# Kernel optimization log

Hardware: AMD Instinct MI355X
Metric: run time of the kernel (lower is better)

Reference implementation:

```python
import jax, jax.numpy as jnp
import numpy as np
from jax import lax


def setup_inputs() -> dict:
    key = jax.random.key(0)
    ks = jax.random.split(key, 6)
    B, L, Cin, N, Cout = 4, 4096, 256, 512, 256
    s = 0.02
    return {
        "x": jax.random.normal(ks[0], (B, L, Cin), dtype=jnp.float32),
        "Wx": jax.random.normal(ks[1], (Cin, N), dtype=jnp.float32) * s,
        "bx": jnp.zeros((N,), dtype=jnp.float32),
        "Wbc": jax.random.normal(ks[2], (Cin, 2 * N), dtype=jnp.float32) * s,
        "bbc": jnp.zeros((2 * N,), dtype=jnp.float32),
        "Wd": jax.random.normal(ks[3], (Cin, N), dtype=jnp.float32) * s,
        "bd": jnp.zeros((N,), dtype=jnp.float32),
        "Wy": jax.random.normal(ks[4], (N, Cout), dtype=jnp.float32) * s,
        "by": jnp.zeros((Cout,), dtype=jnp.float32),
    }


def _scan_combine(c1, c2):
    # linear recurrence h_t = a_t * h_{t-1} + b_t as an associative op
    a1, b1 = c1
    a2, b2 = c2
    return a1 * a2, a2 * b1 + b2


def reference(x, Wx, bx, Wbc, bbc, Wd, bd, Wy, by):
    # projections: [B, L, N]
    x_proj = x @ Wx + bx
    BC = x @ Wbc + bbc
    delta = x @ Wd + bd
    Bm, C = jnp.split(BC, 2, axis=-1)

    A_bar = jnp.exp(-jax.nn.softplus(delta))      # [B, L, N], in (0, 1)
    B_bar = (1.0 - A_bar) * Bm                    # [B, L, N]

    # selective scan (h0 = 0): h_t = A_bar_t * h_{t-1} + B_bar_t * x_proj_t
    u = B_bar * x_proj
    _, h = lax.associative_scan(_scan_combine, (A_bar, u), axis=1)

    y = C * h                                      # [B, L, N]
    return y @ Wy + by                             # [B, L, Cout]
```

## Files before the change

kernel.cpp:

```cpp
#include <hip/hip_runtime.h>
#include <math.h>

constexpr int CIN  = 256;
constexpr int NST  = 512;
constexpr int LSEQ = 4096;
constexpr int BB   = 4;
constexpr int ROWS = BB * LSEQ;
constexpr int COUT = 256;
constexpr int LC   = 64;
constexpr int NC   = LSEQ / LC;

typedef __attribute__((ext_vector_type(8))) short bf16x8;
typedef __attribute__((ext_vector_type(4))) float f32x4;
typedef unsigned short ushort_t;
typedef unsigned int   uint_t;

__device__ __forceinline__ ushort_t f2bf(float f) {
    uint_t u = __float_as_uint(f);
    u = (u + 0x7FFF + ((u >> 16) & 1)) >> 16;
    return (ushort_t)u;
}
__device__ __forceinline__ float bf2f(ushort_t s) {
    return __uint_as_float(((uint_t)s) << 16);
}

__global__ __launch_bounds__(256)
void prep_w_kernel(const float* __restrict__ Wx, const float* __restrict__ Wbc,
                   const float* __restrict__ Wd, const float* __restrict__ Wy,
                   ushort_t* __restrict__ Wt, ushort_t* __restrict__ Wyt)
{
    const int gid = blockIdx.x * 256 + threadIdx.x;
    if (gid < 4 * NST * CIN) {
        const int mat = gid >> 17;
        const int idx = gid & 131071;
        const int k   = idx >> 9;
        const int n   = idx & 511;
        float v;
        if      (mat == 0) v = Wx [k * NST + n];
        else if (mat == 1) v = Wbc[k * (2 * NST) + n];
        else if (mat == 2) v = Wbc[k * (2 * NST) + NST + n];
        else               v = Wd [k * NST + n];
        Wt[((size_t)mat * NST + n) * CIN + k] = f2bf(v);
    } else {
        const int idx = gid - 4 * NST * CIN;
        const int k   = idx >> 8;
        const int n   = idx & 255;
        Wyt[(size_t)n * NST + k] = f2bf(Wy[k * COUT + n]);
    }
}

__global__ __launch_bounds__(256)
void prep_x_kernel(const float* __restrict__ x, ushort_t* __restrict__ xb)
{
    const int i = (blockIdx.x * 256 + threadIdx.x) * 4;
    float4 v = *(const float4*)&x[i];
    uint2 o;
    o.x = (uint_t)f2bf(v.x) | ((uint_t)f2bf(v.y) << 16);
    o.y = (uint_t)f2bf(v.z) | ((uint_t)f2bf(v.w) << 16);
    *(uint2*)&xb[i] = o;
}

__global__ __launch_bounds__(256, 3)
void proj_mfma_kernel(const ushort_t* __restrict__ xb, const ushort_t* __restrict__ Wt,
                      const float* __restrict__ bx, const float* __restrict__ bbc,
                      const float* __restrict__ bd,
                      float* __restrict__ Aarr, float* __restrict__ Uarr,
                      ushort_t* __restrict__ CYb)
{
    __shared__ alignas(16) ushort_t xs[64][72];
    __shared__ alignas(16) ushort_t ws[4][64][72];

    const int tid  = threadIdx.x;
    const int wave = tid >> 6;
    const int lane = tid & 63;
    const int lm   = lane & 15;
    const int lq   = lane >> 4;
    const int row0 = blockIdx.x * 64;
    const int n0   = blockIdx.y * 64;

    const int sr = tid >> 2;
    const int sk = (tid & 3) << 4;

    f32x4 acc[4][4];
    #pragma unroll
    for (int rt = 0; rt < 4; ++rt)
        #pragma unroll
        for (int m = 0; m < 4; ++m)
            acc[rt][m] = (f32x4){0.f, 0.f, 0.f, 0.f};

    const ushort_t* xsrc = xb + (size_t)(row0 + sr) * CIN + sk;
    const ushort_t* wsrc0 = Wt + (size_t)(n0 + sr) * CIN + sk;

    for (int k0 = 0; k0 < CIN; k0 += 64) {
        uint4 xv0 = *(const uint4*)(xsrc + k0);
        uint4 xv1 = *(const uint4*)(xsrc + k0 + 8);
        uint4 wv[4][2];
        #pragma unroll
        for (int m = 0; m < 4; ++m) {
            const ushort_t* p = wsrc0 + (size_t)m * NST * CIN + k0;
            wv[m][0] = *(const uint4*)(p);
            wv[m][1] = *(const uint4*)(p + 8);
        }
        *(uint4*)&xs[sr][sk]     = xv0;
        *(uint4*)&xs[sr][sk + 8] = xv1;
        #pragma unroll
        for (int m = 0; m < 4; ++m) {
            *(uint4*)&ws[m][sr][sk]     = wv[m][0];
            *(uint4*)&ws[m][sr][sk + 8] = wv[m][1];
        }
        __syncthreads();

        #pragma unroll
        for (int ks = 0; ks < 2; ++ks) {
            const int kk = ks * 32 + lq * 8;
            bf16x8 af[4], bf[4];
            #pragma unroll
            for (int rt = 0; rt < 4; ++rt)
                af[rt] = *(const bf16x8*)&xs[rt * 16 + lm][kk];
            #pragma unroll
            for (int m = 0; m < 4; ++m)
                bf[m] = *(const bf16x8*)&ws[m][wave * 16 + lm][kk];
            #pragma unroll
            for (int rt = 0; rt < 4; ++rt)
                #pragma unroll
                for (int m = 0; m < 4; ++m)
                    acc[rt][m] = __builtin_amdgcn_mfma_f32_16x16x32_bf16(
                        af[rt], bf[m], acc[rt][m], 0, 0, 0);
        }
        __syncthreads();
    }

    const int ng = n0 + wave * 16 + lm;
    const float bxv = bx [ng];
    const float bbv = bbc[ng];
    const float bcv = bbc[NST + ng];
    const float bdv = bd [ng];
    #pragma unroll
    for (int rt = 0; rt < 4; ++rt) {
        #pragma unroll
        for (int r = 0; r < 4; ++r) {
            const int row = row0 + rt * 16 + lq * 4 + r;
            float xp = acc[rt][0][r] + bxv;
            float bm = acc[rt][1][r] + bbv;
            float cc = acc[rt][2][r] + bcv;
            float dd = acc[rt][3][r] + bdv;
            dd = fminf(dd, 60.0f);
            float e  = __expf(dd);
            float A  = 1.0f / (1.0f + e);
            float u  = (e * A) * bm * xp;
            const size_t idx = (size_t)row * NST + ng;
            Aarr[idx] = A;
            Uarr[idx] = u;
            CYb[idx]  = f2bf(cc);
        }
    }
}

__global__ __launch_bounds__(256)
void scan_local_kernel(const float* __restrict__ Aarr, const float* __restrict__ Uarr,
                       float* __restrict__ Aprod, float* __restrict__ Hend)
{
    const int gid = blockIdx.x * 256 + threadIdx.x;
    const int n   = gid & (NST - 1);
    const int bc  = gid >> 9;
    const float* Ap = Aarr + (size_t)bc * LC * NST + n;
    const float* Up = Uarr + (size_t)bc * LC * NST + n;
    float ap = 1.0f, h = 0.0f;
    #pragma unroll 8
    for (int t = 0; t < LC; ++t) {
        float a  = Ap[(size_t)t * NST];
        float uu = Up[(size_t)t * NST];
        ap *= a;
        h = fmaf(a, h, uu);
    }
    Aprod[(size_t)bc * NST + n] = ap;
    Hend [(size_t)bc * NST + n] = h;
}

__global__ __launch_bounds__(256)
void scan_carry_kernel(const float* __restrict__ Aprod, const float* __restrict__ Hend,
                       float* __restrict__ Carry)
{
    const int gid = blockIdx.x * 256 + threadIdx.x;
    const int n   = gid & (NST - 1);
    const int b   = gid >> 9;
    float h = 0.0f;
    for (int c = 0; c < NC; ++c) {
        size_t idx = ((size_t)(b * NC + c)) * NST + n;
        Carry[idx] = h;
        h = fmaf(Aprod[idx], h, Hend[idx]);
    }
}

__global__ __launch_bounds__(256)
void scan_final_kernel(const float* __restrict__ Aarr, const float* __restrict__ Uarr,
                       ushort_t* __restrict__ CYb, const float* __restrict__ Carry)
{
    const int gid = blockIdx.x * 256 + threadIdx.x;
    const int n   = gid & (NST - 1);
    const int bc  = gid >> 9;
    const size_t base = (size_t)bc * LC * NST + n;
    float h = Carry[(size_t)bc * NST + n];
    #pragma unroll 8
    for (int t = 0; t < LC; ++t) {
        size_t idx = base + (size_t)t * NST;
        float a  = Aarr[idx];
        float uu = Uarr[idx];
        float cc = bf2f(CYb[idx]);
        h = fmaf(a, h, uu);
        CYb[idx] = f2bf(cc * h);
    }
}

__global__ __launch_bounds__(256, 4)
void out_mfma_kernel(const ushort_t* __restrict__ yb, const ushort_t* __restrict__ Wyt,
                     const float* __restrict__ by, float* __restrict__ out)
{
    __shared__ alignas(16) ushort_t ys [64][72];
    __shared__ alignas(16) ushort_t wys[64][72];

    const int tid  = threadIdx.x;
    const int wave = tid >> 6;
    const int lane = tid & 63;
    const int lm   = lane & 15;
    const int lq   = lane >> 4;
    const int row0 = blockIdx.x * 64;
    const int n0   = blockIdx.y * 64;

    const int sr = tid >> 2;
    const int sk = (tid & 3) << 4;

    f32x4 acc[4];
    #pragma unroll
    for (int rt = 0; rt < 4; ++rt) acc[rt] = (f32x4){0.f, 0.f, 0.f, 0.f};

    const ushort_t* ysrc = yb  + (size_t)(row0 + sr) * NST + sk;
    const ushort_t* wsrc = Wyt + (size_t)(n0  + sr) * NST + sk;

    for (int k0 = 0; k0 < NST; k0 += 64) {
        uint4 yv0 = *(const uint4*)(ysrc + k0);
        uint4 yv1 = *(const uint4*)(ysrc + k0 + 8);
        uint4 wv0 = *(const uint4*)(wsrc + k0);
        uint4 wv1 = *(const uint4*)(wsrc + k0 + 8);
        *(uint4*)&ys [sr][sk]     = yv0;
        *(uint4*)&ys [sr][sk + 8] = yv1;
        *(uint4*)&wys[sr][sk]     = wv0;
        *(uint4*)&wys[sr][sk + 8] = wv1;
        __syncthreads();

        #pragma unroll
        for (int ks = 0; ks < 2; ++ks) {
            const int kk = ks * 32 + lq * 8;
            bf16x8 bfr = *(const bf16x8*)&wys[wave * 16 + lm][kk];
            #pragma unroll
            for (int rt = 0; rt < 4; ++rt) {
                bf16x8 af = *(const bf16x8*)&ys[rt * 16 + lm][kk];
                acc[rt] = __builtin_amdgcn_mfma_f32_16x16x32_bf16(
                    af, bfr, acc[rt], 0, 0, 0);
            }
        }
        __syncthreads();
    }

    const int ng = n0 + wave * 16 + lm;
    const float bv = by[ng];
    #pragma unroll
    for (int rt = 0; rt < 4; ++rt)
        #pragma unroll
        for (int r = 0; r < 4; ++r) {
            const int row = row0 + rt * 16 + lq * 4 + r;
            out[(size_t)row * COUT + ng] = acc[rt][r] + bv;
        }
}

extern "C" void kernel_launch(void* const* d_in, const int* in_sizes, int n_in,
                              void* d_out, int out_size, void* d_ws, size_t ws_size,
                              hipStream_t stream)
{
    const float* x   = (const float*)d_in[0];
    const float* Wx  = (const float*)d_in[1];
    const float* bx  = (const float*)d_in[2];
    const float* Wbc = (const float*)d_in[3];
    const float* bbc = (const float*)d_in[4];
    const float* Wd  = (const float*)d_in[5];
    const float* bd  = (const float*)d_in[6];
    const float* Wy  = (const float*)d_in[7];
    const float* by  = (const float*)d_in[8];
    float* out = (float*)d_out;

    char* p = (char*)d_ws;
    float*    Aarr  = (float*)p;          p += (size_t)ROWS * NST * 4;
    float*    Uarr  = (float*)p;          p += (size_t)ROWS * NST * 4;
    ushort_t* CYb   = (ushort_t*)p;       p += (size_t)ROWS * NST * 2;
    ushort_t* xb    = (ushort_t*)p;       p += (size_t)ROWS * CIN * 2;
    ushort_t* Wt    = (ushort_t*)p;       p += (size_t)4 * NST * CIN * 2;
    ushort_t* Wyt   = (ushort_t*)p;       p += (size_t)COUT * NST * 2;
    float*    Aprod = (float*)p;          p += (size_t)BB * NC * NST * 4;
    float*    Hend  = (float*)p;          p += (size_t)BB * NC * NST * 4;
    float*    Carry = (float*)p;          p += (size_t)BB * NC * NST * 4;

    prep_w_kernel<<<(4 * NST * CIN + COUT * NST) / 256, 256, 0, stream>>>(
        Wx, Wbc, Wd, Wy, Wt, Wyt);

    prep_x_kernel<<<(ROWS * CIN / 4) / 256, 256, 0, stream>>>(x, xb);

    proj_mfma_kernel<<<dim3(ROWS / 64, NST / 64), 256, 0, stream>>>(
        xb, Wt, bx, bbc, bd, Aarr, Uarr, CYb);

    scan_local_kernel<<<(BB * NC * NST) / 256, 256, 0, stream>>>(
        Aarr, Uarr, Aprod, Hend);

    scan_carry_kernel<<<(BB * NST) / 256, 256, 0, stream>>>(
        Aprod, Hend, Carry);

    scan_final_kernel<<<(BB * NC * NST) / 256, 256, 0, stream>>>(
        Aarr, Uarr, CYb, Carry);

    out_mfma_kernel<<<dim3(ROWS / 64, COUT / 64), 256, 0, stream>>>(
        CYb, Wyt, by, out);
}
```

Baseline: 162.5 us.

## Fuse chunk-local scan into projection GEMM and carry correction into output GEMM

New measurement: 208.8 us. 1.28x slower.

```diff
diff --git a/kernel.cpp b/kernel.cpp
--- a/kernel.cpp
+++ b/kernel.cpp
@@ -25,14 +25,24 @@
 }
 
 __global__ __launch_bounds__(256)
-void prep_w_kernel(const float* __restrict__ Wx, const float* __restrict__ Wbc,
-                   const float* __restrict__ Wd, const float* __restrict__ Wy,
-                   ushort_t* __restrict__ Wt, ushort_t* __restrict__ Wyt)
+void prep_kernel(const float* __restrict__ x,
+                 const float* __restrict__ Wx, const float* __restrict__ Wbc,
+                 const float* __restrict__ Wd, const float* __restrict__ Wy,
+                 ushort_t* __restrict__ xb, ushort_t* __restrict__ Wt,
+                 ushort_t* __restrict__ Wyt)
 {
     const int gid = blockIdx.x * 256 + threadIdx.x;
-    if (gid < 4 * NST * CIN) {
-        const int mat = gid >> 17;
-        const int idx = gid & 131071;
+    if (gid < ROWS * CIN / 4) {
+        const int i = gid * 4;
+        float4 v = *(const float4*)&x[i];
+        uint2 o;
+        o.x = (uint_t)f2bf(v.x) | ((uint_t)f2bf(v.y) << 16);
+        o.y = (uint_t)f2bf(v.z) | ((uint_t)f2bf(v.w) << 16);
+        *(uint2*)&xb[i] = o;
+    } else if (gid < ROWS * CIN / 4 + 4 * NST * CIN) {
+        const int wid = gid - ROWS * CIN / 4;
+        const int mat = wid >> 17;
+        const int idx = wid & 131071;
         const int k   = idx >> 9;
         const int n   = idx & 511;
         float v;
@@ -42,33 +52,35 @@
         else               v = Wd [k * NST + n];
         Wt[((size_t)mat * NST + n) * CIN + k] = f2bf(v);
     } else {
-        const int idx = gid - 4 * NST * CIN;
+        const int idx = gid - (ROWS * CIN / 4 + 4 * NST * CIN);
         const int k   = idx >> 8;
         const int n   = idx & 255;
         Wyt[(size_t)n * NST + k] = f2bf(Wy[k * COUT + n]);
     }
 }
 
-__global__ __launch_bounds__(256)
-void prep_x_kernel(const float* __restrict__ x, ushort_t* __restrict__ xb)
-{
-    const int i = (blockIdx.x * 256 + threadIdx.x) * 4;
-    float4 v = *(const float4*)&x[i];
-    uint2 o;
-    o.x = (uint_t)f2bf(v.x) | ((uint_t)f2bf(v.y) << 16);
-    o.y = (uint_t)f2bf(v.z) | ((uint_t)f2bf(v.w) << 16);
-    *(uint2*)&xb[i] = o;
-}
-
 __global__ __launch_bounds__(256, 3)
-void proj_mfma_kernel(const ushort_t* __restrict__ xb, const ushort_t* __restrict__ Wt,
+void proj_scan_kernel(const ushort_t* __restrict__ xb, const ushort_t* __restrict__ Wt,
                       const float* __restrict__ bx, const float* __restrict__ bbc,
                       const float* __restrict__ bd,
-                      float* __restrict__ Aarr, float* __restrict__ Uarr,
-                      ushort_t* __restrict__ CYb)
-{
-    __shared__ alignas(16) ushort_t xs[64][72];
-    __shared__ alignas(16) ushort_t ws[4][64][72];
+                      uint_t* __restrict__ HP,
+                      float* __restrict__ Aprod, float* __restrict__ Hend)
+{
+    __shared__ union {
+        struct {
+            ushort_t xs[64][72];
+            ushort_t ws[4][64][72];
+        } g;
+        struct {
+            float    Als[64][68];
+            float    Uls[64][68];
+            ushort_t Cls[64][72];
+            float    Pseg[4][64];
+            float    Hseg[4][64];
+            float    Cp[4][64];
+            float    Ch[4][64];
+        } s;
+    } sh;
 
     const int tid  = threadIdx.x;
     const int wave = tid >> 6;
@@ -88,7 +100,7 @@
         for (int m = 0; m < 4; ++m)
             acc[rt][m] = (f32x4){0.f, 0.f, 0.f, 0.f};
 
-    const ushort_t* xsrc = xb + (size_t)(row0 + sr) * CIN + sk;
+    const ushort_t* xsrc  = xb + (size_t)(row0 + sr) * CIN + sk;
     const ushort_t* wsrc0 = Wt + (size_t)(n0 + sr) * CIN + sk;
 
     for (int k0 = 0; k0 < CIN; k0 += 64) {
@@ -101,36 +113,39 @@
             wv[m][0] = *(const uint4*)(p);
             wv[m][1] = *(const uint4*)(p + 8);
         }
-        *(uint4*)&xs[sr][sk]     = xv0;
-        *(uint4*)&xs[sr][sk + 8] = xv1;
+        __syncthreads();
+        *(uint4*)&sh.g.xs[sr][sk]     = xv0;
+        *(uint4*)&sh.g.xs[sr][sk + 8] = xv1;
         #pragma unroll
         for (int m = 0; m < 4; ++m) {
-            *(uint4*)&ws[m][sr][sk]     = wv[m][0];
-            *(uint4*)&ws[m][sr][sk + 8] = wv[m][1];
+            *(uint4*)&sh.g.ws[m][sr][sk]     = wv[m][0];
+            *(uint4*)&sh.g.ws[m][sr][sk + 8] = wv[m][1];
         }
         __syncthreads();
 
         #pragma unroll
         for (int ks = 0; ks < 2; ++ks) {
             const int kk = ks * 32 + lq * 8;
-            bf16x8 af[4], bf[4];
+            bf16x8 af[4], bfr[4];
             #pragma unroll
             for (int rt = 0; rt < 4; ++rt)
-                af[rt] = *(const bf16x8*)&xs[rt * 16 + lm][kk];
+                af[rt] = *(const bf16x8*)&sh.g.xs[rt * 16 + lm][kk];
             #pragma unroll
             for (int m = 0; m < 4; ++m)
-                bf[m] = *(const bf16x8*)&ws[m][wave * 16 + lm][kk];
+                bfr[m] = *(const bf16x8*)&sh.g.ws[m][wave * 16 + lm][kk];
             #pragma unroll
             for (int rt = 0; rt < 4; ++rt)
                 #pragma unroll
                 for (int m = 0; m < 4; ++m)
                     acc[rt][m] = __builtin_amdgcn_mfma_f32_16x16x32_bf16(
-                        af[rt], bf[m], acc[rt][m], 0, 0, 0);
-        }
-        __syncthreads();
-    }
-
-    const int ng = n0 + wave * 16 + lm;
+                        af[rt], bfr[m], acc[rt][m], 0, 0, 0);
+        }
+    }
+
+    __syncthreads();
+
+    const int jn = wave * 16 + lm;
+    const int ng = n0 + jn;
     const float bxv = bx [ng];
     const float bbv = bbc[ng];
     const float bcv = bbc[NST + ng];
@@ -139,7 +154,7 @@
     for (int rt = 0; rt < 4; ++rt) {
         #pragma unroll
         for (int r = 0; r < 4; ++r) {
-            const int row = row0 + rt * 16 + lq * 4 + r;
+            const int t = rt * 16 + lq * 4 + r;
             float xp = acc[rt][0][r] + bxv;
             float bm = acc[rt][1][r] + bbv;
             float cc = acc[rt][2][r] + bcv;
@@ -148,33 +163,81 @@
             float e  = __expf(dd);
             float A  = 1.0f / (1.0f + e);
             float u  = (e * A) * bm * xp;
-            const size_t idx = (size_t)row * NST + ng;
-            Aarr[idx] = A;
-            Uarr[idx] = u;
-            CYb[idx]  = f2bf(cc);
-        }
-    }
-}
-
-__global__ __launch_bounds__(256)
-void scan_local_kernel(const float* __restrict__ Aarr, const float* __restrict__ Uarr,
-                       float* __restrict__ Aprod, float* __restrict__ Hend)
-{
-    const int gid = blockIdx.x * 256 + threadIdx.x;
-    const int n   = gid & (NST - 1);
-    const int bc  = gid >> 9;
-    const float* Ap = Aarr + (size_t)bc * LC * NST + n;
-    const float* Up = Uarr + (size_t)bc * LC * NST + n;
-    float ap = 1.0f, h = 0.0f;
-    #pragma unroll 8
-    for (int t = 0; t < LC; ++t) {
-        float a  = Ap[(size_t)t * NST];
-        float uu = Up[(size_t)t * NST];
-        ap *= a;
-        h = fmaf(a, h, uu);
-    }
-    Aprod[(size_t)bc * NST + n] = ap;
-    Hend [(size_t)bc * NST + n] = h;
+            sh.s.Als[t][jn] = A;
+            sh.s.Uls[t][jn] = u;
+            sh.s.Cls[t][jn] = f2bf(cc);
+        }
+    }
+    __syncthreads();
+
+    {
+        const int j = lane, w = wave;
+        float p = 1.0f, h = 0.0f;
+        #pragma unroll
+        for (int i = 0; i < 16; ++i) {
+            const int t = w * 16 + i;
+            float a  = sh.s.Als[t][j];
+            float uu = sh.s.Uls[t][j];
+            h = fmaf(a, h, uu);
+            p *= a;
+            sh.s.Als[t][j] = p;
+            sh.s.Uls[t][j] = h;
+        }
+        sh.s.Pseg[w][j] = p;
+        sh.s.Hseg[w][j] = h;
+    }
+    __syncthreads();
+
+    if (tid < 64) {
+        const int j = tid;
+        float cp = 1.0f, ch = 0.0f;
+        #pragma unroll
+        for (int s = 0; s < 4; ++s) {
+            sh.s.Cp[s][j] = cp;
+            sh.s.Ch[s][j] = ch;
+            float ps = sh.s.Pseg[s][j];
+            float hs = sh.s.Hseg[s][j];
+            ch = fmaf(ps, ch, hs);
+            cp *= ps;
+        }
+        Aprod[(size_t)blockIdx.x * NST + n0 + j] = cp;
+        Hend [(size_t)blockIdx.x * NST + n0 + j] = ch;
+    }
+    __syncthreads();
+
+    {
+        const int j = lane, w = wave;
+        const float cpw = sh.s.Cp[w][j];
+        const float chw = sh.s.Ch[w][j];
+        #pragma unroll
+        for (int i = 0; i < 16; ++i) {
+            const int t = w * 16 + i;
+            float p = sh.s.Als[t][j];
+            float h = sh.s.Uls[t][j];
+            float c = bf2f(sh.s.Cls[t][j]);
+            float hf = fmaf(p, chw, h);
+            float pf = p * cpw;
+            uint_t g1 = f2bf(c * hf);
+            uint_t g2 = f2bf(c * pf);
+            ((uint_t*)&sh.s.Uls[t][0])[j] = (g2 << 16) | g1;
+        }
+    }
+    __syncthreads();
+
+    {
+        const int r  = tid >> 2;
+        const int nq = (tid & 3) * 16;
+        const uint_t* src = (const uint_t*)&sh.s.Uls[r][0] + nq;
+        uint_t* dst = HP + (size_t)(row0 + r) * NST + n0 + nq;
+        uint4 v0 = *(const uint4*)(src);
+        uint4 v1 = *(const uint4*)(src + 4);
+        uint4 v2 = *(const uint4*)(src + 8);
+        uint4 v3 = *(const uint4*)(src + 12);
+        *(uint4*)(dst)      = v0;
+        *(uint4*)(dst + 4)  = v1;
+        *(uint4*)(dst + 8)  = v2;
+        *(uint4*)(dst + 12) = v3;
+    }
 }
 
 __global__ __launch_bounds__(256)
@@ -192,29 +255,10 @@
     }
 }
 
-__global__ __launch_bounds__(256)
-void scan_final_kernel(const float* __restrict__ Aarr, const float* __restrict__ Uarr,
-                       ushort_t* __restrict__ CYb, const float* __restrict__ Carry)
-{
-    const int gid = blockIdx.x * 256 + threadIdx.x;
-    const int n   = gid & (NST - 1);
-    const int bc  = gid >> 9;
-    const size_t base = (size_t)bc * LC * NST + n;
-    float h = Carry[(size_t)bc * NST + n];
-    #pragma unroll 8
-    for (int t = 0; t < LC; ++t) {
-        size_t idx = base + (size_t)t * NST;
-        float a  = Aarr[idx];
-        float uu = Uarr[idx];
-        float cc = bf2f(CYb[idx]);
-        h = fmaf(a, h, uu);
-        CYb[idx] = f2bf(cc * h);
-    }
-}
-
 __global__ __launch_bounds__(256, 4)
-void out_mfma_kernel(const ushort_t* __restrict__ yb, const ushort_t* __restrict__ Wyt,
-                     const float* __restrict__ by, float* __restrict__ out)
+void out_fused_kernel(const uint_t* __restrict__ HP, const float* __restrict__ Carry,
+                      const ushort_t* __restrict__ Wyt, const float* __restrict__ by,
+                      float* __restrict__ out)
 {
     __shared__ alignas(16) ushort_t ys [64][72];
     __shared__ alignas(16) ushort_t wys[64][72];
@@ -234,16 +278,38 @@
     #pragma unroll
     for (int rt = 0; rt < 4; ++rt) acc[rt] = (f32x4){0.f, 0.f, 0.f, 0.f};
 
-    const ushort_t* ysrc = yb  + (size_t)(row0 + sr) * NST + sk;
+    const uint_t*   hsrc = HP  + (size_t)(row0 + sr) * NST + sk;
     const ushort_t* wsrc = Wyt + (size_t)(n0  + sr) * NST + sk;
+    const float*    carr = Carry + (size_t)blockIdx.x * NST + sk;
 
     for (int k0 = 0; k0 < NST; k0 += 64) {
-        uint4 yv0 = *(const uint4*)(ysrc + k0);
-        uint4 yv1 = *(const uint4*)(ysrc + k0 + 8);
+        uint4 hv[4];
+        #pragma unroll
+        for (int q = 0; q < 4; ++q) hv[q] = *(const uint4*)(hsrc + k0 + q * 4);
+        float4 cv[4];
+        #pragma unroll
+        for (int q = 0; q < 4; ++q) cv[q] = *(const float4*)(carr + k0 + q * 4);
         uint4 wv0 = *(const uint4*)(wsrc + k0);
         uint4 wv1 = *(const uint4*)(wsrc + k0 + 8);
-        *(uint4*)&ys [sr][sk]     = yv0;
-        *(uint4*)&ys [sr][sk + 8] = yv1;
+
+        uint_t yo[8];
+        #pragma unroll
+        for (int q = 0; q < 4; ++q) {
+            const float* cvp = (const float*)&cv[q];
+            const uint_t* hvp = (const uint_t*)&hv[q];
+            #pragma unroll
+            for (int e = 0; e < 4; e += 2) {
+                uint_t pk0 = hvp[e], pk1 = hvp[e + 1];
+                float y0 = fmaf(bf2f((ushort_t)(pk0 >> 16)), cvp[e],
+                                bf2f((ushort_t)(pk0 & 0xffff)));
+                float y1 = fmaf(bf2f((ushort_t)(pk1 >> 16)), cvp[e + 1],
+                                bf2f((ushort_t)(pk1 & 0xffff)));
+                yo[q * 2 + e / 2] = (uint_t)f2bf(y0) | ((uint_t)f2bf(y1) << 16);
+            }
+        }
+        __syncthreads();
+        *(uint4*)&ys[sr][sk]      = *(uint4*)&yo[0];
+        *(uint4*)&ys[sr][sk + 8]  = *(uint4*)&yo[4];
         *(uint4*)&wys[sr][sk]     = wv0;
         *(uint4*)&wys[sr][sk + 8] = wv1;
         __syncthreads();
@@ -259,7 +325,6 @@
                     af, bfr, acc[rt], 0, 0, 0);
             }
         }
-        __syncthreads();
     }
 
     const int ng = n0 + wave * 16 + lm;
@@ -289,9 +354,7 @@
     float* out = (float*)d_out;
 
     char* p = (char*)d_ws;
-    float*    Aarr  = (float*)p;          p += (size_t)ROWS * NST * 4;
-    float*    Uarr  = (float*)p;          p += (size_t)ROWS * NST * 4;
-    ushort_t* CYb   = (ushort_t*)p;       p += (size_t)ROWS * NST * 2;
+    uint_t*   HP    = (uint_t*)p;         p += (size_t)ROWS * NST * 4;
     ushort_t* xb    = (ushort_t*)p;       p += (size_t)ROWS * CIN * 2;
     ushort_t* Wt    = (ushort_t*)p;       p += (size_t)4 * NST * CIN * 2;
     ushort_t* Wyt   = (ushort_t*)p;       p += (size_t)COUT * NST * 2;
@@ -299,23 +362,16 @@
     float*    Hend  = (float*)p;          p += (size_t)BB * NC * NST * 4;
     float*    Carry = (float*)p;          p += (size_t)BB * NC * NST * 4;
 
-    prep_w_kernel<<<(4 * NST * CIN + COUT * NST) / 256, 256, 0, stream>>>(
-        Wx, Wbc, Wd, Wy, Wt, Wyt);
-
-    prep_x_kernel<<<(ROWS * CIN / 4) / 256, 256, 0, stream>>>(x, xb);
-
-    proj_mfma_kernel<<<dim3(ROWS / 64, NST / 64), 256, 0, stream>>>(
-        xb, Wt, bx, bbc, bd, Aarr, Uarr, CYb);
-
-    scan_local_kernel<<<(BB * NC * NST) / 256, 256, 0, stream>>>(
-        Aarr, Uarr, Aprod, Hend);
+    const int prep_threads = ROWS * CIN / 4 + 4 * NST * CIN + COUT * NST;
+    prep_kernel<<<prep_threads / 256, 256, 0, stream>>>(
+        x, Wx, Wbc, Wd, Wy, xb, Wt, Wyt);
+
+    proj_scan_kernel<<<dim3(ROWS / 64, NST / 64), 256, 0, stream>>>(
+        xb, Wt, bx, bbc, bd, HP, Aprod, Hend);
 
     scan_carry_kernel<<<(BB * NST) / 256, 256, 0, stream>>>(
         Aprod, Hend, Carry);
 
-    scan_final_kernel<<<(BB * NC * NST) / 256, 256, 0, stream>>>(
-        Aarr, Uarr, CYb, Carry);
-
-    out_mfma_kernel<<<dim3(ROWS / 64, COUT / 64), 256, 0, stream>>>(
-        CYb, Wyt, by, out);
-}
+    out_fused_kernel<<<dim3(ROWS / 64, COUT / 64), 256, 0, stream>>>(
+        HP, Carry, Wyt, by, out);
+}
```

## Fuse chunk-local scan into projection epilogue and merge prep kernels

Applied to the files above, without the earlier changes.

Measured after the change: 207.9 us. 27.9% more time.

```diff
diff --git a/kernel.cpp b/kernel.cpp
--- a/kernel.cpp
+++ b/kernel.cpp
@@ -25,14 +25,24 @@
 }
 
 __global__ __launch_bounds__(256)
-void prep_w_kernel(const float* __restrict__ Wx, const float* __restrict__ Wbc,
-                   const float* __restrict__ Wd, const float* __restrict__ Wy,
-                   ushort_t* __restrict__ Wt, ushort_t* __restrict__ Wyt)
+void prep_kernel(const float* __restrict__ x,
+                 const float* __restrict__ Wx, const float* __restrict__ Wbc,
+                 const float* __restrict__ Wd, const float* __restrict__ Wy,
+                 ushort_t* __restrict__ xb, ushort_t* __restrict__ Wt,
+                 ushort_t* __restrict__ Wyt)
 {
     const int gid = blockIdx.x * 256 + threadIdx.x;
-    if (gid < 4 * NST * CIN) {
-        const int mat = gid >> 17;
-        const int idx = gid & 131071;
+    if (gid < ROWS * CIN / 4) {
+        const int i = gid * 4;
+        float4 v = *(const float4*)&x[i];
+        uint2 o;
+        o.x = (uint_t)f2bf(v.x) | ((uint_t)f2bf(v.y) << 16);
+        o.y = (uint_t)f2bf(v.z) | ((uint_t)f2bf(v.w) << 16);
+        *(uint2*)&xb[i] = o;
+    } else if (gid < ROWS * CIN / 4 + 4 * NST * CIN) {
+        const int wid = gid - ROWS * CIN / 4;
+        const int mat = wid >> 17;
+        const int idx = wid & 131071;
         const int k   = idx >> 9;
         const int n   = idx & 511;
         float v;
@@ -42,22 +52,11 @@
         else               v = Wd [k * NST + n];
         Wt[((size_t)mat * NST + n) * CIN + k] = f2bf(v);
     } else {
-        const int idx = gid - 4 * NST * CIN;
+        const int idx = gid - (ROWS * CIN / 4 + 4 * NST * CIN);
         const int k   = idx >> 8;
         const int n   = idx & 255;
         Wyt[(size_t)n * NST + k] = f2bf(Wy[k * COUT + n]);
     }
-}
-
-__global__ __launch_bounds__(256)
-void prep_x_kernel(const float* __restrict__ x, ushort_t* __restrict__ xb)
-{
-    const int i = (blockIdx.x * 256 + threadIdx.x) * 4;
-    float4 v = *(const float4*)&x[i];
-    uint2 o;
-    o.x = (uint_t)f2bf(v.x) | ((uint_t)f2bf(v.y) << 16);
-    o.y = (uint_t)f2bf(v.z) | ((uint_t)f2bf(v.w) << 16);
-    *(uint2*)&xb[i] = o;
 }
 
 __global__ __launch_bounds__(256, 3)
@@ -65,7 +64,8 @@
                       const float* __restrict__ bx, const float* __restrict__ bbc,
                       const float* __restrict__ bd,
                       float* __restrict__ Aarr, float* __restrict__ Uarr,
-                      ushort_t* __restrict__ CYb)
+                      ushort_t* __restrict__ CYb,
+                      float* __restrict__ Aprod, float* __restrict__ Hend)
 {
     __shared__ alignas(16) ushort_t xs[64][72];
     __shared__ alignas(16) ushort_t ws[4][64][72];
@@ -88,7 +88,7 @@
         for (int m = 0; m < 4; ++m)
             acc[rt][m] = (f32x4){0.f, 0.f, 0.f, 0.f};
 
-    const ushort_t* xsrc = xb + (size_t)(row0 + sr) * CIN + sk;
+    const ushort_t* xsrc  = xb + (size_t)(row0 + sr) * CIN + sk;
     const ushort_t* wsrc0 = Wt + (size_t)(n0 + sr) * CIN + sk;
 
     for (int k0 = 0; k0 < CIN; k0 += 64) {
@@ -101,6 +101,7 @@
             wv[m][0] = *(const uint4*)(p);
             wv[m][1] = *(const uint4*)(p + 8);
         }
+        __syncthreads();
         *(uint4*)&xs[sr][sk]     = xv0;
         *(uint4*)&xs[sr][sk + 8] = xv1;
         #pragma unroll
@@ -113,21 +114,20 @@
         #pragma unroll
         for (int ks = 0; ks < 2; ++ks) {
             const int kk = ks * 32 + lq * 8;
-            bf16x8 af[4], bf[4];
+            bf16x8 af[4], bfr[4];
             #pragma unroll
             for (int rt = 0; rt < 4; ++rt)
                 af[rt] = *(const bf16x8*)&xs[rt * 16 + lm][kk];
             #pragma unroll
             for (int m = 0; m < 4; ++m)
-                bf[m] = *(const bf16x8*)&ws[m][wave * 16 + lm][kk];
+                bfr[m] = *(const bf16x8*)&ws[m][wave * 16 + lm][kk];
             #pragma unroll
             for (int rt = 0; rt < 4; ++rt)
                 #pragma unroll
                 for (int m = 0; m < 4; ++m)
                     acc[rt][m] = __builtin_amdgcn_mfma_f32_16x16x32_bf16(
-                        af[rt], bf[m], acc[rt][m], 0, 0, 0);
-        }
-        __syncthreads();
+                        af[rt], bfr[m], acc[rt][m], 0, 0, 0);
+        }
     }
 
     const int ng = n0 + wave * 16 + lm;
@@ -135,8 +135,11 @@
     const float bbv = bbc[ng];
     const float bcv = bbc[NST + ng];
     const float bdv = bd [ng];
+
+    float P4[4], H4[4];
     #pragma unroll
     for (int rt = 0; rt < 4; ++rt) {
+        float p = 1.0f, h = 0.0f;
         #pragma unroll
         for (int r = 0; r < 4; ++r) {
             const int row = row0 + rt * 16 + lq * 4 + r;
@@ -152,29 +155,38 @@
             Aarr[idx] = A;
             Uarr[idx] = u;
             CYb[idx]  = f2bf(cc);
-        }
-    }
-}
-
-__global__ __launch_bounds__(256)
-void scan_local_kernel(const float* __restrict__ Aarr, const float* __restrict__ Uarr,
-                       float* __restrict__ Aprod, float* __restrict__ Hend)
-{
-    const int gid = blockIdx.x * 256 + threadIdx.x;
-    const int n   = gid & (NST - 1);
-    const int bc  = gid >> 9;
-    const float* Ap = Aarr + (size_t)bc * LC * NST + n;
-    const float* Up = Uarr + (size_t)bc * LC * NST + n;
-    float ap = 1.0f, h = 0.0f;
-    #pragma unroll 8
-    for (int t = 0; t < LC; ++t) {
-        float a  = Ap[(size_t)t * NST];
-        float uu = Up[(size_t)t * NST];
-        ap *= a;
-        h = fmaf(a, h, uu);
-    }
-    Aprod[(size_t)bc * NST + n] = ap;
-    Hend [(size_t)bc * NST + n] = h;
+            h = fmaf(A, h, u);
+            p *= A;
+        }
+        P4[rt] = p;
+        H4[rt] = h;
+    }
+
+    float TP[4], TH[4];
+    #pragma unroll
+    for (int rt = 0; rt < 4; ++rt) {
+        float iP = P4[rt], iH = H4[rt];
+        float tP = __shfl_up(iP, 16, 64);
+        float tH = __shfl_up(iH, 16, 64);
+        if (lq >= 1) { iH = fmaf(iP, tH, iH); iP *= tP; }
+        tP = __shfl_up(iP, 32, 64);
+        tH = __shfl_up(iH, 32, 64);
+        if (lq >= 2) { iH = fmaf(iP, tH, iH); iP *= tP; }
+        TP[rt] = __shfl(iP, 48 + lm, 64);
+        TH[rt] = __shfl(iH, 48 + lm, 64);
+    }
+
+    float bP = 1.0f, bH = 0.0f;
+    #pragma unroll
+    for (int rt = 0; rt < 4; ++rt) {
+        bH = fmaf(TP[rt], bH, TH[rt]);
+        bP *= TP[rt];
+    }
+    if (lq == 0) {
+        const size_t sidx = (size_t)blockIdx.x * NST + ng;
+        Aprod[sidx] = bP;
+        Hend [sidx] = bH;
+    }
 }
 
 __global__ __launch_bounds__(256)
@@ -242,6 +254,7 @@
         uint4 yv1 = *(const uint4*)(ysrc + k0 + 8);
         uint4 wv0 = *(const uint4*)(wsrc + k0);
         uint4 wv1 = *(const uint4*)(wsrc + k0 + 8);
+        __syncthreads();
         *(uint4*)&ys [sr][sk]     = yv0;
         *(uint4*)&ys [sr][sk + 8] = yv1;
         *(uint4*)&wys[sr][sk]     = wv0;
@@ -259,7 +272,6 @@
                     af, bfr, acc[rt], 0, 0, 0);
             }
         }
-        __syncthreads();
     }
 
     const int ng = n0 + wave * 16 + lm;
@@ -299,16 +311,12 @@
     float*    Hend  = (float*)p;          p += (size_t)BB * NC * NST * 4;
     float*    Carry = (float*)p;          p += (size_t)BB * NC * NST * 4;
 
-    prep_w_kernel<<<(4 * NST * CIN + COUT * NST) / 256, 256, 0, stream>>>(
-        Wx, Wbc, Wd, Wy, Wt, Wyt);
-
-    prep_x_kernel<<<(ROWS * CIN / 4) / 256, 256, 0, stream>>>(x, xb);
+    const int prep_threads = ROWS * CIN / 4 + 4 * NST * CIN + COUT * NST;
+    prep_kernel<<<prep_threads / 256, 256, 0, stream>>>(
+        x, Wx, Wbc, Wd, Wy, xb, Wt, Wyt);
 
     proj_mfma_kernel<<<dim3(ROWS / 64, NST / 64), 256, 0, stream>>>(
-        xb, Wt, bx, bbc, bd, Aarr, Uarr, CYb);
-
-    scan_local_kernel<<<(BB * NC * NST) / 256, 256, 0, stream>>>(
-        Aarr, Uarr, Aprod, Hend);
+        xb, Wt, bx, bbc, bd, Aarr, Uarr, CYb, Aprod, Hend);
 
     scan_carry_kernel<<<(BB * NST) / 256, 256, 0, stream>>>(
         Aprod, Hend, Carry);
```

## Fuse x fp32-to-bf16 conversion into projection GEMM and move barriers before LDS stores

Applied to the files above, without the earlier changes.

New measurement: 229.6 us. 41.2% more time.

```diff
diff --git a/kernel.cpp b/kernel.cpp
--- a/kernel.cpp
+++ b/kernel.cpp
@@ -22,6 +22,9 @@
 }
 __device__ __forceinline__ float bf2f(ushort_t s) {
     return __uint_as_float(((uint_t)s) << 16);
+}
+__device__ __forceinline__ uint_t pack2bf(float a, float b) {
+    return (uint_t)f2bf(a) | ((uint_t)f2bf(b) << 16);
 }
 
 __global__ __launch_bounds__(256)
@@ -49,19 +52,8 @@
     }
 }
 
-__global__ __launch_bounds__(256)
-void prep_x_kernel(const float* __restrict__ x, ushort_t* __restrict__ xb)
-{
-    const int i = (blockIdx.x * 256 + threadIdx.x) * 4;
-    float4 v = *(const float4*)&x[i];
-    uint2 o;
-    o.x = (uint_t)f2bf(v.x) | ((uint_t)f2bf(v.y) << 16);
-    o.y = (uint_t)f2bf(v.z) | ((uint_t)f2bf(v.w) << 16);
-    *(uint2*)&xb[i] = o;
-}
-
 __global__ __launch_bounds__(256, 3)
-void proj_mfma_kernel(const ushort_t* __restrict__ xb, const ushort_t* __restrict__ Wt,
+void proj_mfma_kernel(const float* __restrict__ x, const ushort_t* __restrict__ Wt,
                       const float* __restrict__ bx, const float* __restrict__ bbc,
                       const float* __restrict__ bd,
                       float* __restrict__ Aarr, float* __restrict__ Uarr,
@@ -88,12 +80,14 @@
         for (int m = 0; m < 4; ++m)
             acc[rt][m] = (f32x4){0.f, 0.f, 0.f, 0.f};
 
-    const ushort_t* xsrc = xb + (size_t)(row0 + sr) * CIN + sk;
+    const float*    xsrc  = x  + (size_t)(row0 + sr) * CIN + sk;
     const ushort_t* wsrc0 = Wt + (size_t)(n0 + sr) * CIN + sk;
 
     for (int k0 = 0; k0 < CIN; k0 += 64) {
-        uint4 xv0 = *(const uint4*)(xsrc + k0);
-        uint4 xv1 = *(const uint4*)(xsrc + k0 + 8);
+        float4 a0 = *(const float4*)(xsrc + k0);
+        float4 a1 = *(const float4*)(xsrc + k0 + 4);
+        float4 a2 = *(const float4*)(xsrc + k0 + 8);
+        float4 a3 = *(const float4*)(xsrc + k0 + 12);
         uint4 wv[4][2];
         #pragma unroll
         for (int m = 0; m < 4; ++m) {
@@ -101,6 +95,13 @@
             wv[m][0] = *(const uint4*)(p);
             wv[m][1] = *(const uint4*)(p + 8);
         }
+        uint4 xv0, xv1;
+        xv0.x = pack2bf(a0.x, a0.y); xv0.y = pack2bf(a0.z, a0.w);
+        xv0.z = pack2bf(a1.x, a1.y); xv0.w = pack2bf(a1.z, a1.w);
+        xv1.x = pack2bf(a2.x, a2.y); xv1.y = pack2bf(a2.z, a2.w);
+        xv1.z = pack2bf(a3.x, a3.y); xv1.w = pack2bf(a3.z, a3.w);
+
+        __syncthreads();
         *(uint4*)&xs[sr][sk]     = xv0;
         *(uint4*)&xs[sr][sk + 8] = xv1;
         #pragma unroll
@@ -113,21 +114,20 @@
         #pragma unroll
         for (int ks = 0; ks < 2; ++ks) {
             const int kk = ks * 32 + lq * 8;
-            bf16x8 af[4], bf[4];
+            bf16x8 af[4], bfr[4];
             #pragma unroll
             for (int rt = 0; rt < 4; ++rt)
                 af[rt] = *(const bf16x8*)&xs[rt * 16 + lm][kk];
             #pragma unroll
             for (int m = 0; m < 4; ++m)
-                bf[m] = *(const bf16x8*)&ws[m][wave * 16 + lm][kk];
+                bfr[m] = *(const bf16x8*)&ws[m][wave * 16 + lm][kk];
             #pragma unroll
             for (int rt = 0; rt < 4; ++rt)
                 #pragma unroll
                 for (int m = 0; m < 4; ++m)
                     acc[rt][m] = __builtin_amdgcn_mfma_f32_16x16x32_bf16(
-                        af[rt], bf[m], acc[rt][m], 0, 0, 0);
-        }
-        __syncthreads();
+                        af[rt], bfr[m], acc[rt][m], 0, 0, 0);
+        }
     }
 
     const int ng = n0 + wave * 16 + lm;
@@ -242,6 +242,7 @@
         uint4 yv1 = *(const uint4*)(ysrc + k0 + 8);
         uint4 wv0 = *(const uint4*)(wsrc + k0);
         uint4 wv1 = *(const uint4*)(wsrc + k0 + 8);
+        __syncthreads();
         *(uint4*)&ys [sr][sk]     = yv0;
         *(uint4*)&ys [sr][sk + 8] = yv1;
         *(uint4*)&wys[sr][sk]     = wv0;
@@ -259,7 +260,6 @@
                     af, bfr, acc[rt], 0, 0, 0);
             }
         }
-        __syncthreads();
     }
 
     const int ng = n0 + wave * 16 + lm;
@@ -292,7 +292,6 @@
     float*    Aarr  = (float*)p;          p += (size_t)ROWS * NST * 4;
     float*    Uarr  = (float*)p;          p += (size_t)ROWS * NST * 4;
     ushort_t* CYb   = (ushort_t*)p;       p += (size_t)ROWS * NST * 2;
-    ushort_t* xb    = (ushort_t*)p;       p += (size_t)ROWS * CIN * 2;
     ushort_t* Wt    = (ushort_t*)p;       p += (size_t)4 * NST * CIN * 2;
     ushort_t* Wyt   = (ushort_t*)p;       p += (size_t)COUT * NST * 2;
     float*    Aprod = (float*)p;          p += (size_t)BB * NC * NST * 4;
@@ -302,10 +301,8 @@
     prep_w_kernel<<<(4 * NST * CIN + COUT * NST) / 256, 256, 0, stream>>>(
         Wx, Wbc, Wd, Wy, Wt, Wyt);
 
-    prep_x_kernel<<<(ROWS * CIN / 4) / 256, 256, 0, stream>>>(x, xb);
-
     proj_mfma_kernel<<<dim3(ROWS / 64, NST / 64), 256, 0, stream>>>(
-        xb, Wt, bx, bbc, bd, Aarr, Uarr, CYb);
+        x, Wt, bx, bbc, bd, Aarr, Uarr, CYb);
 
     scan_local_kernel<<<(BB * NC * NST) / 256, 256, 0, stream>>>(
         Aarr, Uarr, Aprod, Hend);
```
